# Kernel optimization log

Hardware: AMD Instinct MI355X
Metric: run time of the kernel (lower is better)

Reference implementation:

```python
import jax, jax.numpy as jnp
import numpy as np

N = 100000      # nodes
E = 640000      # edges
IN = 100        # in_channels
OUT = 128       # out_channels
H, D = 4, 32    # heads, per-head dim (OUT = H*D)
MSG, TOUT, ETD, NET = 16, 100, 8, 4
EDGE_COLS = MSG + TOUT + 2        # 118 raw edge_attr columns
EDIM = (MSG - 1) + ETD + TOUT + 2 # 125 processed edge feature dim
SCALE = 1.0 / np.sqrt(D)


def _lin(k, fi, fo):
    return (jax.random.normal(k, (fi, fo), jnp.float32) / np.sqrt(fi)).astype(jnp.float32)


def setup_inputs() -> dict:
    key = jax.random.key(0)
    ks = jax.random.split(key, 24)
    x = jax.random.normal(ks[0], (N, IN), jnp.float32)
    edge_index = jax.random.randint(ks[1], (2, E), 0, N, dtype=jnp.int32)
    ea = jax.random.normal(ks[2], (E, EDGE_COLS), jnp.float32)
    etype = jax.random.randint(ks[3], (E,), 0, NET).astype(jnp.float32)
    edge_attr = ea.at[:, 3].set(etype)
    emb = jax.random.normal(ks[4], (NET, ETD), jnp.float32)
    inp = {"x": x, "edge_index": edge_index, "edge_attr": edge_attr, "emb": emb}
    # conv1: in=IN, conv2: in=OUT; lin_edge has no bias (PyG default)
    for i, fi in ((1, IN), (2, OUT)):
        base = 5 + (i - 1) * 8
        inp[f"w{i}q"] = _lin(ks[base + 0], fi, OUT)
        inp[f"b{i}q"] = jnp.zeros((OUT,), jnp.float32)
        inp[f"w{i}k"] = _lin(ks[base + 1], fi, OUT)
        inp[f"b{i}k"] = jnp.zeros((OUT,), jnp.float32)
        inp[f"w{i}v"] = _lin(ks[base + 2], fi, OUT)
        inp[f"b{i}v"] = jnp.zeros((OUT,), jnp.float32)
        inp[f"w{i}e"] = _lin(ks[base + 3], EDIM, OUT)
        inp[f"w{i}s"] = _lin(ks[base + 4], fi, OUT)
        inp[f"b{i}s"] = jnp.zeros((OUT,), jnp.float32)
    return inp


def _seg_softmax(logits, seg, n):
    # logits: [E, H], softmax over edges sharing the same target node
    m = jax.ops.segment_max(logits, seg, num_segments=n)      # [N, H]
    ex = jnp.exp(logits - m[seg])
    s = jax.ops.segment_sum(ex, seg, num_segments=n)          # [N, H]
    return ex / (s[seg] + 1e-16)


def _tconv(x, src, dst, e, wq, bq, wk, bk, wv, bv, we, ws, bs):
    n = x.shape[0]
    q = (x @ wq + bq)[dst].reshape(-1, H, D)   # gather targets
    k = (x @ wk + bk)[src].reshape(-1, H, D)   # gather sources
    v = (x @ wv + bv)[src].reshape(-1, H, D)
    ee = (e @ we).reshape(-1, H, D)            # per-edge projection
    alpha = jnp.sum(q * (k + ee), axis=-1) * SCALE          # [E, H]
    a = _seg_softmax(alpha, dst, n)                          # scatter-softmax
    msg = (v + ee) * a[..., None]                            # [E, H, D]
    out = jax.ops.segment_sum(msg, dst, num_segments=n).reshape(n, H * D)
    return out + x @ ws + bs                                 # root/skip connection


def reference(x, edge_index, edge_attr, emb,
              w1q, b1q, w1k, b1k, w1v, b1v, w1e, w1s, b1s,
              w2q, b2q, w2k, b2k, w2v, b2v, w2e, w2s, b2s):
    src, dst = edge_index[0], edge_index[1]
    cont = edge_attr[:, :3]
    etype = edge_attr[:, 3].astype(jnp.int32)
    rest = edge_attr[:, 4:]
    e = jnp.concatenate([cont, rest, emb[etype]], axis=-1)   # [E, EDIM]
    h = jax.nn.relu(_tconv(x, src, dst, e, w1q, b1q, w1k, b1k, w1v, b1v, w1e, w1s, b1s))
    return _tconv(h, src, dst, e, w2q, b2q, w2k, b2k, w2v, b2v, w2e, w2s, b2s)
```

## Files before the change

### kernel.cpp

```cpp
#include <hip/hip_runtime.h>

#define NN 100000
#define NE 640000
#define OUTF 128
#define K1 100
#define KE 118
#define KPAD 128
#define ASTR 136
#define ATT_SCALE 0.17677669529663687f
#define NSCANB 391

typedef __attribute__((ext_vector_type(8))) short short8;
typedef __attribute__((ext_vector_type(4))) float f32x4;

__device__ __forceinline__ unsigned short f2bf(float f) {
    unsigned u = __float_as_uint(f);
    u += 0x7FFFu + ((u >> 16) & 1u);
    return (unsigned short)(u >> 16);
}
__device__ __forceinline__ float bf2f(unsigned short h) {
    return __uint_as_float(((unsigned)h) << 16);
}

__global__ void prep_weights(
    const float* __restrict__ w1q, const float* __restrict__ w1k,
    const float* __restrict__ w1v, const float* __restrict__ w1s,
    const float* __restrict__ w2q, const float* __restrict__ w2k,
    const float* __restrict__ w2v, const float* __restrict__ w2s,
    const float* __restrict__ we1, const float* __restrict__ we2,
    const float* __restrict__ emb,
    const float* __restrict__ b1q, const float* __restrict__ b1k,
    const float* __restrict__ b1v, const float* __restrict__ b1s,
    const float* __restrict__ b2q, const float* __restrict__ b2k,
    const float* __restrict__ b2v, const float* __restrict__ b2s,
    unsigned short* __restrict__ WT1, unsigned short* __restrict__ WT2,
    unsigned short* __restrict__ WmT1, unsigned short* __restrict__ WmT2,
    float* __restrict__ bias1, float* __restrict__ bias2)
{
    int idx = blockIdx.x * blockDim.x + threadIdx.x;
    int stride = gridDim.x * blockDim.x;
    for (int i = idx; i < 512 * KPAD; i += stride) {
        int col = i >> 7, k = i & 127;
        int which = col >> 7, c = col & 127;
        const float* s1 = (which == 0) ? w1q : (which == 1) ? w1k : (which == 2) ? w1v : w1s;
        const float* s2 = (which == 0) ? w2q : (which == 1) ? w2k : (which == 2) ? w2v : w2s;
        float v1 = (k < K1) ? s1[k * OUTF + c] : 0.f;
        float v2 = s2[k * OUTF + c];
        WT1[i] = f2bf(v1); WT2[i] = f2bf(v2);
    }
    for (int i = idx; i < OUTF * KPAD; i += stride) {
        int col = i >> 7, k = i & 127;
        float v1 = 0.f, v2 = 0.f;
        if (k < 3)                 { v1 = we1[k * OUTF + col];       v2 = we2[k * OUTF + col]; }
        else if (k >= 4 && k < KE) { v1 = we1[(k - 1) * OUTF + col]; v2 = we2[(k - 1) * OUTF + col]; }
        else if (k >= KE && k < KE + 4) {
            int t = k - KE;
            #pragma unroll
            for (int r = 0; r < 8; r++) {
                float ev = emb[t * 8 + r];
                v1 += ev * we1[(117 + r) * OUTF + col];
                v2 += ev * we2[(117 + r) * OUTF + col];
            }
        }
        WmT1[i] = f2bf(v1); WmT2[i] = f2bf(v2);
    }
    for (int i = idx; i < 512; i += stride) {
        int which = i >> 7, c = i & 127;
        const float* sb1 = (which == 0) ? b1q : (which == 1) ? b1k : (which == 2) ? b1v : b1s;
        const float* sb2 = (which == 0) ? b2q : (which == 1) ? b2k : (which == 2) ? b2v : b2s;
        bias1[i] = sb1[c]; bias2[i] = sb2[c];
    }
}

__global__ void hist_kernel(const int* __restrict__ dstI, int* __restrict__ cnt) {
    int e = blockIdx.x * 256 + threadIdx.x;
    if (e < NE) atomicAdd(&cnt[dstI[e]], 1);
}
__global__ void scan1(const int* __restrict__ cnt, int* __restrict__ S1, int* __restrict__ bsum) {
    __shared__ int sd[256];
    int t = blockIdx.x * 256 + threadIdx.x;
    sd[threadIdx.x] = (t < NN) ? cnt[t] : 0;
    __syncthreads();
    for (int off = 1; off < 256; off <<= 1) {
        int x = (threadIdx.x >= off) ? sd[threadIdx.x - off] : 0;
        __syncthreads();
        sd[threadIdx.x] += x;
        __syncthreads();
    }
    if (t < NN) S1[t] = sd[threadIdx.x];
    if (threadIdx.x == 255) bsum[blockIdx.x] = sd[255];
}
__global__ void scan2(const int* __restrict__ bsum, int* __restrict__ boff) {
    __shared__ int sd[512];
    int t = threadIdx.x;
    sd[t] = (t < NSCANB) ? bsum[t] : 0;
    __syncthreads();
    for (int off = 1; off < 512; off <<= 1) {
        int x = (t >= off) ? sd[t - off] : 0;
        __syncthreads();
        sd[t] += x;
        __syncthreads();
    }
    if (t < NSCANB) boff[t] = (t == 0) ? 0 : sd[t - 1];
}
__global__ void scan3(const int* __restrict__ S1, const int* __restrict__ boff,
                      const int* __restrict__ cnt,
                      int* __restrict__ row_start, int* __restrict__ cursor) {
    int t = blockIdx.x * 256 + threadIdx.x;
    if (t < NN) {
        int incl = S1[t] + boff[t >> 8];
        row_start[t + 1] = incl;
        cursor[t] = incl - cnt[t];
        if (t == 0) row_start[0] = 0;
    }
}
__global__ void scatter_csr(const int* __restrict__ srcI, const int* __restrict__ dstI,
                            int* __restrict__ cursor,
                            int* __restrict__ csr_src, int* __restrict__ csr_eid) {
    int e = blockIdx.x * 256 + threadIdx.x;
    if (e < NE) {
        int j = atomicAdd(&cursor[dstI[e]], 1);
        csr_src[j] = srcI[e];
        csr_eid[j] = e;
    }
}

__global__ __launch_bounds__(256) void node_mfma(
    const float* __restrict__ X, int ldx, int Kdim, int relu, int n,
    const unsigned short* __restrict__ WT, const float* __restrict__ bias,
    float* __restrict__ Qp, unsigned short* __restrict__ KVp, float* __restrict__ Hp)
{
    __shared__ unsigned short Alds[128][ASTR];
    int tid = threadIdx.x;
    int rowbase = (blockIdx.x >> 2) * 128;
    int nb = blockIdx.x & 3;

    for (int idx = tid; idx < 128 * 68; idx += 256) {
        int r = idx / 68, kv = idx % 68;
        int k = kv * 2;
        float2 v = make_float2(0.f, 0.f);
        int gr = rowbase + r;
        if (gr < n && k < Kdim) v = *(const float2*)(X + (size_t)gr * ldx + k);
        if (relu) { v.x = fmaxf(v.x, 0.f); v.y = fmaxf(v.y, 0.f); }
        unsigned pv = (unsigned)f2bf(v.x) | ((unsigned)f2bf(v.y) << 16);
        *(unsigned*)&Alds[r][k] = pv;
    }
    __syncthreads();

    int lane = tid & 63, wid = tid >> 6;
    int wm = wid >> 1, wn = wid & 1;
    int l15 = lane & 15, l4 = lane >> 4;

    f32x4 acc[4][4];
    #pragma unroll
    for (int mf = 0; mf < 4; mf++)
        #pragma unroll
        for (int nf = 0; nf < 4; nf++)
            acc[mf][nf] = (f32x4){0.f, 0.f, 0.f, 0.f};

    const unsigned short* wbase = WT + (size_t)(nb * 128 + wn * 64 + l15) * KPAD + l4 * 8;
    #pragma unroll
    for (int ks = 0; ks < 4; ks++) {
        short8 af[4], bfr[4];
        #pragma unroll
        for (int mf = 0; mf < 4; mf++)
            af[mf] = *(const short8*)&Alds[wm * 64 + mf * 16 + l15][ks * 32 + l4 * 8];
        #pragma unroll
        for (int nf = 0; nf < 4; nf++)
            bfr[nf] = *(const short8*)(wbase + (size_t)nf * 16 * KPAD + ks * 32);
        #pragma unroll
        for (int mf = 0; mf < 4; mf++)
            #pragma unroll
            for (int nf = 0; nf < 4; nf++)
                acc[mf][nf] = __builtin_amdgcn_mfma_f32_16x16x32_bf16(af[mf], bfr[nf], acc[mf][nf], 0, 0, 0);
    }
    __syncthreads();

    if (nb == 1 || nb == 2) {
        #pragma unroll
        for (int nf = 0; nf < 4; nf++) {
            int col = wn * 64 + nf * 16 + l15;
            float bv = bias[nb * 128 + col];
            #pragma unroll
            for (int mf = 0; mf < 4; mf++)
                #pragma unroll
                for (int rr = 0; rr < 4; rr++)
                    Alds[wm * 64 + mf * 16 + l4 * 4 + rr][col] = f2bf(acc[mf][nf][rr] + bv);
        }
        __syncthreads();
        int off = (nb == 1) ? 0 : 128;
        #pragma unroll
        for (int it = 0; it < 8; it++) {
            int idx = it * 256 + tid;
            int row = idx >> 4, c8 = (idx & 15) * 8;
            if (rowbase + row < n) {
                uint4 v = *(const uint4*)&Alds[row][c8];
                *(uint4*)(KVp + (size_t)(rowbase + row) * 256 + off + c8) = v;
            }
        }
    } else {
        float* Yp = (nb == 0) ? Qp : Hp;
        float scale = (nb == 0) ? ATT_SCALE : 1.f;
        float (*Sf)[68] = (float (*)[68])Alds;
        #pragma unroll
        for (int h = 0; h < 2; h++) {
            if (wn == h) {
                #pragma unroll
                for (int nf = 0; nf < 4; nf++) {
                    int col = wn * 64 + nf * 16 + l15;
                    float bv = bias[nb * 128 + col];
                    #pragma unroll
                    for (int mf = 0; mf < 4; mf++)
                        #pragma unroll
                        for (int rr = 0; rr < 4; rr++)
                            Sf[wm * 64 + mf * 16 + l4 * 4 + rr][nf * 16 + l15] =
                                (acc[mf][nf][rr] + bv) * scale;
                }
            }
            __syncthreads();
            #pragma unroll
            for (int it = 0; it < 8; it++) {
                int idx = it * 256 + tid;
                int row = idx >> 4, c4 = (idx & 15) * 4;
                if (rowbase + row < n) {
                    float4 v = *(const float4*)&Sf[row][c4];
                    *(float4*)(Yp + (size_t)(rowbase + row) * OUTF + h * 64 + c4) = v;
                }
            }
            if (h == 0) __syncthreads();
        }
    }
}

__global__ __launch_bounds__(256) void edge_mfma_fused(
    const float* __restrict__ EA,
    const unsigned short* __restrict__ WmT1, const unsigned short* __restrict__ WmT2,
    unsigned short* __restrict__ EE1, unsigned short* __restrict__ EE2)
{
    __shared__ unsigned short Tlds[64][ASTR];
    int tid = threadIdx.x;
    int lane = tid & 63, w = tid >> 6;
    int e0 = blockIdx.x * 64;
    int l15 = lane & 15, l4 = lane >> 4;
    int rbase = w * 16;
    const float* rp = EA + (size_t)(e0 + rbase + l15) * KE;

    int et = (int)rp[3];
    int oh = KE + et;

    short8 af[4];
    #pragma unroll
    for (int ks = 0; ks < 4; ks++) {
        int cbase = ks * 32 + l4 * 8;
        float f[8];
        #pragma unroll
        for (int h = 0; h < 4; h++) {
            int c = cbase + h * 2;
            float2 t = make_float2(0.f, 0.f);
            if (c + 2 <= KE) t = *(const float2*)(rp + c);
            f[h * 2] = t.x; f[h * 2 + 1] = t.y;
        }
        #pragma unroll
        for (int j = 0; j < 8; j++) {
            int col = cbase + j;
            float fv = (col == 3) ? 0.f : f[j];
            unsigned short bs = f2bf(fv);
            if (ks == 3 && col == oh) bs = 0x3F80;
            af[ks][j] = bs;
        }
    }

    auto do_layer = [&](const unsigned short* __restrict__ WmT, unsigned short* __restrict__ EEc) {
        f32x4 acc[8];
        #pragma unroll
        for (int nf = 0; nf < 8; nf++) acc[nf] = (f32x4){0.f, 0.f, 0.f, 0.f};

        #pragma unroll
        for (int ks = 0; ks < 4; ks++) {
            short8 bfr[8];
            #pragma unroll
            for (int nf = 0; nf < 8; nf++)
                bfr[nf] = *(const short8*)(WmT + (size_t)(nf * 16 + l15) * KPAD + ks * 32 + l4 * 8);
            #pragma unroll
            for (int nf = 0; nf < 8; nf++)
                acc[nf] = __builtin_amdgcn_mfma_f32_16x16x32_bf16(af[ks], bfr[nf], acc[nf], 0, 0, 0);
        }
        #pragma unroll
        for (int nf = 0; nf < 8; nf++)
            #pragma unroll
            for (int rr = 0; rr < 4; rr++)
                Tlds[rbase + l4 * 4 + rr][nf * 16 + l15] = f2bf(acc[nf][rr]);
        #pragma unroll
        for (int it = 0; it < 4; it++) {
            int t2 = it * 64 + lane;
            int rid = t2 >> 4, c8 = (t2 & 15) * 8;
            uint4 v = *(const uint4*)&Tlds[rbase + rid][c8];
            *(uint4*)(EEc + ((size_t)(e0 + rbase + rid)) * 128 + c8) = v;
        }
    };
    do_layer(WmT1, EE1);
    do_layer(WmT2, EE2);
}

__global__ __launch_bounds__(256) void attn_node(
    const float* __restrict__ Qp, const unsigned short* __restrict__ KVp,
    const unsigned short* __restrict__ EEc,
    const int* __restrict__ row_start, const int* __restrict__ csr_src,
    const int* __restrict__ csr_eid,
    const float* __restrict__ Hskip, float* __restrict__ Out)
{
    int lane = threadIdx.x & 63;
    int gw = (int)((blockIdx.x * (size_t)blockDim.x + threadIdx.x) >> 6);
    int nW = (gridDim.x * blockDim.x) >> 6;
    int c2 = lane * 2;

    for (int d = gw; d < NN; d += nW) {
        int rs = row_start[d], re = row_start[d + 1];
        float2 q = *(const float2*)(Qp + (size_t)d * OUTF + c2);
        float m = -3.4e38f, s = 0.f, a0 = 0.f, a1 = 0.f;

        int j0 = (rs < re) ? rs : 0;
        int sj = csr_src[j0];
        int ej = csr_eid[j0];
        unsigned kc = *(const unsigned*)(KVp + (size_t)sj * 256 + c2);
        unsigned vc = *(const unsigned*)(KVp + (size_t)sj * 256 + 128 + c2);
        unsigned ec = *(const unsigned*)(EEc + (size_t)ej * 128 + c2);

        for (int j = rs; j < re; j++) {
            int jn = (j + 1 < re) ? j + 1 : j;
            int sjn = csr_src[jn];
            int ejn = csr_eid[jn];
            unsigned kn = *(const unsigned*)(KVp + (size_t)sjn * 256 + c2);
            unsigned vn = *(const unsigned*)(KVp + (size_t)sjn * 256 + 128 + c2);
            unsigned en = *(const unsigned*)(EEc + (size_t)ejn * 128 + c2);

            float e0 = bf2f((unsigned short)(ec & 0xFFFFu));
            float e1 = bf2f((unsigned short)(ec >> 16));
            float k0 = bf2f((unsigned short)(kc & 0xFFFFu));
            float k1 = bf2f((unsigned short)(kc >> 16));
            float v0 = bf2f((unsigned short)(vc & 0xFFFFu));
            float v1 = bf2f((unsigned short)(vc >> 16));

            float t = q.x * (k0 + e0) + q.y * (k1 + e1);
            t += __shfl_xor(t, 1); t += __shfl_xor(t, 2);
            t += __shfl_xor(t, 4); t += __shfl_xor(t, 8);
            float alpha = t;
            float mn = fmaxf(m, alpha);
            float r = __expf(m - mn);
            float p = __expf(alpha - mn);
            s = s * r + p;
            a0 = a0 * r + p * (v0 + e0);
            a1 = a1 * r + p * (v1 + e1);
            m = mn;
            kc = kn; vc = vn; ec = en;
        }
        float inv = 1.f / (s + 1e-16f);
        float2 h = *(const float2*)(Hskip + (size_t)d * OUTF + c2);
        float2 o;
        o.x = a0 * inv + h.x;
        o.y = a1 * inv + h.y;
        *(float2*)(Out + (size_t)d * OUTF + c2) = o;
    }
}

extern "C" void kernel_launch(void* const* d_in, const int* in_sizes, int n_in,
                              void* d_out, int out_size, void* d_ws, size_t ws_size,
                              hipStream_t stream) {
    const float* x    = (const float*)d_in[0];
    const int*   ei   = (const int*)d_in[1];
    const float* ea   = (const float*)d_in[2];
    const float* emb  = (const float*)d_in[3];
    const float* w1q  = (const float*)d_in[4];  const float* b1q = (const float*)d_in[5];
    const float* w1k  = (const float*)d_in[6];  const float* b1k = (const float*)d_in[7];
    const float* w1v  = (const float*)d_in[8];  const float* b1v = (const float*)d_in[9];
    const float* w1e  = (const float*)d_in[10];
    const float* w1s  = (const float*)d_in[11]; const float* b1s = (const float*)d_in[12];
    const float* w2q  = (const float*)d_in[13]; const float* b2q = (const float*)d_in[14];
    const float* w2k  = (const float*)d_in[15]; const float* b2k = (const float*)d_in[16];
    const float* w2v  = (const float*)d_in[17]; const float* b2v = (const float*)d_in[18];
    const float* w2e  = (const float*)d_in[19];
    const float* w2s  = (const float*)d_in[20]; const float* b2s = (const float*)d_in[21];

    const int* srcI = ei;
    const int* dstI = ei + NE;

    float* Q = (float*)d_ws;
    unsigned short* KV = (unsigned short*)(Q + (size_t)NN * OUTF);
    float* H = (float*)(KV + (size_t)NN * 256);
    unsigned short* EE1 = (unsigned short*)(H + (size_t)NN * OUTF);
    unsigned short* EE2 = EE1 + (size_t)NE * 128;
    int* csr_src   = (int*)(EE2 + (size_t)NE * 128);
    int* csr_eid   = csr_src + NE;
    int* row_start = csr_eid + NE;
    int* cursor    = row_start + NN + 1;
    int* cnt       = cursor + NN;
    int* S1        = cnt + NN;
    int* bsum      = S1 + NN;
    int* boff      = bsum + NSCANB;
    unsigned short* WT1  = (unsigned short*)(boff + NSCANB + 1);
    unsigned short* WT2  = WT1 + 512 * KPAD;
    unsigned short* WmT1 = WT2 + 512 * KPAD;
    unsigned short* WmT2 = WmT1 + OUTF * KPAD;
    float* bias1 = (float*)(WmT2 + OUTF * KPAD);
    float* bias2 = bias1 + 512;

    prep_weights<<<128, 256, 0, stream>>>(w1q, w1k, w1v, w1s, w2q, w2k, w2v, w2s,
                                          w1e, w2e, emb,
                                          b1q, b1k, b1v, b1s, b2q, b2k, b2v, b2s,
                                          WT1, WT2, WmT1, WmT2, bias1, bias2);
    hipMemsetAsync(cnt, 0, (size_t)NN * sizeof(int), stream);
    hist_kernel<<<NE / 256, 256, 0, stream>>>(dstI, cnt);
    scan1<<<NSCANB, 256, 0, stream>>>(cnt, S1, bsum);
    scan2<<<1, 512, 0, stream>>>(bsum, boff);
    scan3<<<NSCANB, 256, 0, stream>>>(S1, boff, cnt, row_start, cursor);
    scatter_csr<<<NE / 256, 256, 0, stream>>>(srcI, dstI, cursor, csr_src, csr_eid);

    int ngrid = ((NN + 127) / 128) * 4;
    int egrid = NE / 64;

    node_mfma<<<ngrid, 256, 0, stream>>>(x, K1, K1, 0, NN, WT1, bias1, Q, KV, H);
    edge_mfma_fused<<<egrid, 256, 0, stream>>>(ea, WmT1, WmT2, EE1, EE2);
    attn_node<<<2048, 256, 0, stream>>>(Q, KV, EE1, row_start, csr_src, csr_eid, H, H);

    node_mfma<<<ngrid, 256, 0, stream>>>(H, OUTF, OUTF, 1, NN, WT2, bias2, Q, KV, (float*)d_out);
    attn_node<<<2048, 256, 0, stream>>>(Q, KV, EE2, row_start, csr_src, csr_eid, (float*)d_out, (float*)d_out);
}
```

Measured before the change: 1.061 ms.

## Process multiple edge tiles per block with prefetch; deepen CSR index prefetch in attention

```diff
diff --git a/kernel.cpp b/kernel.cpp
--- a/kernel.cpp
+++ b/kernel.cpp
@@ -9,6 +9,7 @@
 #define ASTR 136
 #define ATT_SCALE 0.17677669529663687f
 #define NSCANB 391
+#define ETILES 5
 
 typedef __attribute__((ext_vector_type(8))) short short8;
 typedef __attribute__((ext_vector_type(4))) float f32x4;
@@ -240,37 +241,43 @@
     __shared__ unsigned short Tlds[64][ASTR];
     int tid = threadIdx.x;
     int lane = tid & 63, w = tid >> 6;
-    int e0 = blockIdx.x * 64;
     int l15 = lane & 15, l4 = lane >> 4;
     int rbase = w * 16;
-    const float* rp = EA + (size_t)(e0 + rbase + l15) * KE;
-
-    int et = (int)rp[3];
-    int oh = KE + et;
-
-    short8 af[4];
-    #pragma unroll
-    for (int ks = 0; ks < 4; ks++) {
-        int cbase = ks * 32 + l4 * 8;
-        float f[8];
-        #pragma unroll
-        for (int h = 0; h < 4; h++) {
-            int c = cbase + h * 2;
-            float2 t = make_float2(0.f, 0.f);
-            if (c + 2 <= KE) t = *(const float2*)(rp + c);
-            f[h * 2] = t.x; f[h * 2 + 1] = t.y;
-        }
-        #pragma unroll
-        for (int j = 0; j < 8; j++) {
-            int col = cbase + j;
-            float fv = (col == 3) ? 0.f : f[j];
-            unsigned short bs = f2bf(fv);
-            if (ks == 3 && col == oh) bs = 0x3F80;
-            af[ks][j] = bs;
-        }
-    }
-
-    auto do_layer = [&](const unsigned short* __restrict__ WmT, unsigned short* __restrict__ EEc) {
+    int tile0 = blockIdx.x * ETILES;
+
+    auto load_raw = [&](int tile, float2* f, float& etf) {
+        const float* rp = EA + (size_t)(tile * 64 + rbase + l15) * KE;
+        etf = rp[3];
+        #pragma unroll
+        for (int ks = 0; ks < 4; ks++) {
+            int cbase = ks * 32 + l4 * 8;
+            #pragma unroll
+            for (int h = 0; h < 4; h++) {
+                int c = cbase + h * 2;
+                float2 t = make_float2(0.f, 0.f);
+                if (c + 2 <= KE) t = *(const float2*)(rp + c);
+                f[ks * 4 + h] = t;
+            }
+        }
+    };
+    auto convert = [&](const float2* f, float etf, short8* af) {
+        int oh = KE + (int)etf;
+        #pragma unroll
+        for (int ks = 0; ks < 4; ks++) {
+            int cbase = ks * 32 + l4 * 8;
+            #pragma unroll
+            for (int j = 0; j < 8; j++) {
+                int col = cbase + j;
+                float fv = (j & 1) ? f[ks * 4 + (j >> 1)].y : f[ks * 4 + (j >> 1)].x;
+                if (col == 3) fv = 0.f;
+                unsigned short bs = f2bf(fv);
+                if (ks == 3 && col == oh) bs = 0x3F80;
+                af[ks][j] = bs;
+            }
+        }
+    };
+    auto do_layer = [&](const unsigned short* __restrict__ WmT, unsigned short* __restrict__ EEc,
+                        int e0, const short8* af) {
         f32x4 acc[8];
         #pragma unroll
         for (int nf = 0; nf < 8; nf++) acc[nf] = (f32x4){0.f, 0.f, 0.f, 0.f};
@@ -298,8 +305,23 @@
             *(uint4*)(EEc + ((size_t)(e0 + rbase + rid)) * 128 + c8) = v;
         }
     };
-    do_layer(WmT1, EE1);
-    do_layer(WmT2, EE2);
+
+    float2 fraw[16];
+    float etf;
+    short8 af[4];
+    load_raw(tile0, fraw, etf);
+    convert(fraw, etf, af);
+
+    #pragma unroll
+    for (int t = 0; t < ETILES; t++) {
+        int e0 = (tile0 + t) * 64;
+        do_layer(WmT1, EE1, e0, af);
+        float2 fnext[16];
+        float etn = 0.f;
+        if (t + 1 < ETILES) load_raw(tile0 + t + 1, fnext, etn);
+        do_layer(WmT2, EE2, e0, af);
+        if (t + 1 < ETILES) convert(fnext, etn, af);
+    }
 }
 
 __global__ __launch_bounds__(256) void attn_node(
@@ -320,19 +342,20 @@
         float m = -3.4e38f, s = 0.f, a0 = 0.f, a1 = 0.f;
 
         int j0 = (rs < re) ? rs : 0;
-        int sj = csr_src[j0];
-        int ej = csr_eid[j0];
-        unsigned kc = *(const unsigned*)(KVp + (size_t)sj * 256 + c2);
-        unsigned vc = *(const unsigned*)(KVp + (size_t)sj * 256 + 128 + c2);
-        unsigned ec = *(const unsigned*)(EEc + (size_t)ej * 128 + c2);
+        int jlast = (rs < re) ? re - 1 : 0;
+        int sjA = csr_src[j0], ejA = csr_eid[j0];
+        int j1 = (j0 + 1 <= jlast) ? j0 + 1 : jlast;
+        int sjB = csr_src[j1], ejB = csr_eid[j1];
+        unsigned kc = *(const unsigned*)(KVp + (size_t)sjA * 256 + c2);
+        unsigned vc = *(const unsigned*)(KVp + (size_t)sjA * 256 + 128 + c2);
+        unsigned ec = *(const unsigned*)(EEc + (size_t)ejA * 128 + c2);
 
         for (int j = rs; j < re; j++) {
-            int jn = (j + 1 < re) ? j + 1 : j;
-            int sjn = csr_src[jn];
-            int ejn = csr_eid[jn];
-            unsigned kn = *(const unsigned*)(KVp + (size_t)sjn * 256 + c2);
-            unsigned vn = *(const unsigned*)(KVp + (size_t)sjn * 256 + 128 + c2);
-            unsigned en = *(const unsigned*)(EEc + (size_t)ejn * 128 + c2);
+            unsigned kn = *(const unsigned*)(KVp + (size_t)sjB * 256 + c2);
+            unsigned vn = *(const unsigned*)(KVp + (size_t)sjB * 256 + 128 + c2);
+            unsigned en = *(const unsigned*)(EEc + (size_t)ejB * 128 + c2);
+            int j2 = (j + 2 <= jlast) ? j + 2 : jlast;
+            int sjC = csr_src[j2], ejC = csr_eid[j2];
 
             float e0 = bf2f((unsigned short)(ec & 0xFFFFu));
             float e1 = bf2f((unsigned short)(ec >> 16));
@@ -353,6 +376,7 @@
             a1 = a1 * r + p * (v1 + e1);
             m = mn;
             kc = kn; vc = vn; ec = en;
+            sjB = sjC; ejB = ejC;
         }
         float inv = 1.f / (s + 1e-16f);
         float2 h = *(const float2*)(Hskip + (size_t)d * OUTF + c2);
@@ -416,7 +440,7 @@
     scatter_csr<<<NE / 256, 256, 0, stream>>>(srcI, dstI, cursor, csr_src, csr_eid);
 
     int ngrid = ((NN + 127) / 128) * 4;
-    int egrid = NE / 64;
+    int egrid = NE / (64 * ETILES);
 
     node_mfma<<<ngrid, 256, 0, stream>>>(x, K1, K1, 0, NN, WT1, bias1, Q, KV, H);
     edge_mfma_fused<<<egrid, 256, 0, stream>>>(ea, WmT1, WmT2, EE1, EE2);
```

Measured after the change: 994.1 us. -6.3%, faster.
